# Optimization experiments

Hardware: AMD Instinct MI355X
Metric: run time of the kernel (lower is better)

Reference implementation:

```python
import jax, jax.numpy as jnp
import numpy as np

T = 2048        # num tokens
HID = 2048      # hidden_size
HQ = 16         # num_heads
HKV = 8         # num_kv_heads
D = 128         # head_dim
P = 2           # power retention exponent
THETA = 10000.0 # rope base
SCALE = D ** -0.5


def setup_inputs() -> dict:
    key = jax.random.key(0)
    ks = jax.random.split(key, 8)
    s = 0.02
    return {
        "positions": jnp.arange(T, dtype=jnp.int64) if jax.config.jax_enable_x64 else jnp.arange(T, dtype=jnp.int32),
        "hidden_states": jax.random.normal(ks[0], (T, HID), jnp.float32),
        "Wq": jax.random.normal(ks[1], (HID, HQ * D), jnp.float32) * s,
        "bq": jnp.zeros((HQ * D,), jnp.float32),
        "Wk": jax.random.normal(ks[2], (HID, HKV * D), jnp.float32) * s,
        "bk": jnp.zeros((HKV * D,), jnp.float32),
        "Wv": jax.random.normal(ks[3], (HID, HKV * D), jnp.float32) * s,
        "bv": jnp.zeros((HKV * D,), jnp.float32),
        "Wg": jax.random.normal(ks[4], (HID, HKV), jnp.float32) * s,
        "bg": jnp.zeros((HKV,), jnp.float32),
        "Wo": jax.random.normal(ks[5], (HQ * D, HID), jnp.float32) * s,
        "bo": jnp.zeros((HID,), jnp.float32),
    }


def _rope_neox(x, pos):
    # x: [T, H, D], pos: [T]; rotate-half (neox) style, rotary_dim == head_dim
    half = D // 2
    inv_freq = 1.0 / (THETA ** (jnp.arange(0, D, 2, dtype=jnp.float32) / D))  # [D/2]
    freqs = pos.astype(jnp.float32)[:, None] * inv_freq                        # [T, D/2]
    cos = jnp.cos(freqs)[:, None, :]
    sin = jnp.sin(freqs)[:, None, :]
    x1, x2 = x[..., :half], x[..., half:]
    return jnp.concatenate([x1 * cos - x2 * sin, x2 * cos + x1 * sin], axis=-1)


def reference(positions, hidden_states, Wq, bq, Wk, bk, Wv, bv, Wg, bg, Wo, bo):
    # QKVG projections
    q = (hidden_states @ Wq + bq).reshape(T, HQ, D)
    k = (hidden_states @ Wk + bk).reshape(T, HKV, D)
    v = (hidden_states @ Wv + bv).reshape(T, HKV, D)
    g = hidden_states @ Wg + bg            # [T, HKV], one gate scalar per kv head

    # RoPE on q/k, logsigmoid gate in fp32
    q = _rope_neox(q, positions)
    k = _rope_neox(k, positions)
    g = jax.nn.log_sigmoid(g.astype(jnp.float32))   # [T, HKV], <= 0
    G = jnp.cumsum(g, axis=0)                       # [T, HKV] cumulative log-decay

    # GQA: expand kv heads to query heads
    rep = HQ // HKV
    k = jnp.repeat(k, rep, axis=1)   # [T, HQ, D]
    v = jnp.repeat(v, rep, axis=1)
    G = jnp.repeat(G, rep, axis=1)   # [T, HQ]

    # Power retention (quadratic attention form, seq_len <= switch_over_seq_len):
    # W_ij = (scale * q_i . k_j)^p * exp(G_i - G_j), causal j <= i
    S = jnp.einsum('thd,shd->hts', q, k) * SCALE      # [H, T, T]
    S = S ** P
    Gh = G.T                                          # [H, T]
    mask = jnp.tril(jnp.ones((T, T), dtype=bool))
    diff = jnp.where(mask[None], Gh[:, :, None] - Gh[:, None, :], -jnp.inf)
    W = S * jnp.exp(diff)                             # decay<=1 inside mask, 0 outside

    out = jnp.einsum('hts,shd->thd', W, v)            # [T, H, D]
    out = out.reshape(T, HQ * D) @ Wo + bo            # o_proj
    return out
```

## Files before the change

kernel.cpp:

```cpp
#include <hip/hip_runtime.h>
#include <hip/hip_bf16.h>
#include <math.h>

#define T_SEQ 2048
#define HID 2048
#define HQ 16
#define HKV 8
#define D_HEAD 128
#define HALF 64
#define SCALE_F 0.08838834764831845f
#define PROJW 4096

typedef __attribute__((ext_vector_type(8))) short bf16x8;
typedef __attribute__((ext_vector_type(4))) float f32x4;

static __device__ __forceinline__ short f2bf(float x) {
  unsigned u = __builtin_bit_cast(unsigned, x);
  unsigned r = (u + 0x7FFF + ((u >> 16) & 1)) >> 16;
  return (short)r;
}
static __device__ __forceinline__ float bf2f(unsigned short u) {
  unsigned v = ((unsigned)u) << 16;
  return __builtin_bit_cast(float, v);
}

#define GLDS(gsrc, ldst) \
  __builtin_amdgcn_global_load_lds((const __attribute__((address_space(1))) void*)(gsrc), \
                                   (__attribute__((address_space(3))) void*)(ldst), 16, 0, 0)

__global__ __launch_bounds__(256)
void transpose_qkvw(const float* __restrict__ Wq, const float* __restrict__ Wk,
                    const float* __restrict__ Wv, short* __restrict__ BTall)
{
  const int bx = blockIdx.x;
  const int k0 = blockIdx.y * 32;
  const float* src; short* dst; int Nsrc, n0;
  if (bx < 64)       { src = Wq; Nsrc = 2048; dst = BTall;                       n0 = bx * 32; }
  else if (bx < 96)  { src = Wk; Nsrc = 1024; dst = BTall + (size_t)2048 * 2048; n0 = (bx - 64) * 32; }
  else               { src = Wv; Nsrc = 1024; dst = BTall + (size_t)3072 * 2048; n0 = (bx - 96) * 32; }

  __shared__ float tile[32][33];
  const int r = threadIdx.x >> 5, c = threadIdx.x & 31;
  #pragma unroll
  for (int i = 0; i < 4; ++i)
    tile[r + i * 8][c] = src[(size_t)(k0 + r + i * 8) * Nsrc + n0 + c];
  __syncthreads();
  const int n = threadIdx.x >> 3, k4 = (threadIdx.x & 7) * 4;
  short4 o;
  o.x = f2bf(tile[k4 + 0][n]); o.y = f2bf(tile[k4 + 1][n]);
  o.z = f2bf(tile[k4 + 2][n]); o.w = f2bf(tile[k4 + 3][n]);
  *reinterpret_cast<short4*>(&dst[(size_t)(n0 + n) * 2048 + k0 + k4]) = o;
}

__global__ __launch_bounds__(256)
void transpose_wo(const float* __restrict__ Wo, short* __restrict__ WoT)
{
  const int k0 = blockIdx.y * 32, n0 = blockIdx.x * 32;
  __shared__ float tile[32][33];
  const int r = threadIdx.x >> 5, c = threadIdx.x & 31;
  #pragma unroll
  for (int i = 0; i < 4; ++i)
    tile[r + i * 8][c] = Wo[(size_t)(k0 + r + i * 8) * 2048 + n0 + c];
  __syncthreads();
  const int n = threadIdx.x >> 3, k4 = (threadIdx.x & 7) * 4;
  short4 o;
  o.x = f2bf(tile[k4 + 0][n]); o.y = f2bf(tile[k4 + 1][n]);
  o.z = f2bf(tile[k4 + 2][n]); o.w = f2bf(tile[k4 + 3][n]);
  *reinterpret_cast<short4*>(&WoT[(size_t)(n0 + n) * 2048 + k0 + k4]) = o;
}

template <bool OBF0>
__global__ __launch_bounds__(512, 1)
void gemm256(const short* __restrict__ A, const short* __restrict__ BT,
             const float* __restrict__ b0, const float* __restrict__ b1,
             const float* __restrict__ b2, int s1, int s2,
             void* __restrict__ C0, short* __restrict__ P1,
             short* __restrict__ P2, short* __restrict__ P3,
             int N, int Kst, int klen)
{
  __shared__ __align__(16) short Al[2][256 * 64];
  __shared__ __align__(16) short Bl[2][256 * 64];
  const int tid = threadIdx.x, wid = tid >> 6, lane = tid & 63;
  const int z = blockIdx.z, koff = z * klen;
  const int nwg = gridDim.x * gridDim.y;
  const int orig = blockIdx.y * gridDim.x + blockIdx.x;
  const int swz = (orig & 7) * (nwg >> 3) + (orig >> 3);
  const int bx = swz % gridDim.x, by = swz / gridDim.x;
  const int bm0 = by * 256, bn0 = bx * 256;
  const int wr = wid >> 2, wc = wid & 3;
  const int c = lane & 15, g = lane >> 4;
  const int xc = (c & 7) << 4;
  const int nk = klen >> 6;

  f32x4 acc[8][4] = {};

#define STGA(p, kt, j) do {                                                   \
    const int cid = (j) * 512 + tid;                                          \
    const int rr = cid >> 3;                                                  \
    const int gx = (cid & 7) ^ (rr & 7);                                      \
    GLDS(A + (size_t)(bm0 + rr) * Kst + koff + (kt) * 64 + gx * 8,            \
         (char*)&Al[p][0] + ((j) * 512 + wid * 64) * 16);                     \
  } while (0)
#define STGB(p, kt, j) do {                                                   \
    const int cid = (j) * 512 + tid;                                          \
    const int rr = cid >> 3;                                                  \
    const int gx = (cid & 7) ^ (rr & 7);                                      \
    GLDS(BT + (size_t)(bn0 + rr) * Kst + koff + (kt) * 64 + gx * 8,           \
         (char*)&Bl[p][0] + ((j) * 512 + wid * 64) * 16);                     \
  } while (0)
#define STAGE(p, kt) do {                                                     \
    STGA(p, kt, 0); STGA(p, kt, 1); STGA(p, kt, 2); STGA(p, kt, 3);           \
    STGB(p, kt, 0); STGB(p, kt, 1); STGB(p, kt, 2); STGB(p, kt, 3);           \
  } while (0)

#define RDA(p, mf, ks)                                                        \
  (*reinterpret_cast<const bf16x8*>((const char*)&Al[p][0] +                  \
      (size_t)(wr * 128 + (mf) * 16 + c) * 128 + (((ks) * 64 + g * 16) ^ xc)))
#define RDB(p, nf, ks)                                                        \
  (*reinterpret_cast<const bf16x8*>((const char*)&Bl[p][0] +                  \
      (size_t)(wc * 64 + (nf) * 16 + c) * 128 + (((ks) * 64 + g * 16) ^ xc)))

  STAGE(0, 0);
  asm volatile("s_waitcnt vmcnt(0)" ::: "memory");
  __builtin_amdgcn_s_barrier();
  __builtin_amdgcn_sched_barrier(0);

  for (int t = 0; t < nk; ++t) {
    const int p = t & 1;
    if (t + 1 < nk) STAGE(p ^ 1, t + 1);

    {
      bf16x8 af[8], bfr[4];
      #pragma unroll
      for (int mf = 0; mf < 8; ++mf) af[mf] = RDA(p, mf, 0);
      #pragma unroll
      for (int nf = 0; nf < 4; ++nf) bfr[nf] = RDB(p, nf, 0);
      asm volatile("s_waitcnt lgkmcnt(0)" ::: "memory");
      __builtin_amdgcn_sched_barrier(0);
      __builtin_amdgcn_s_setprio(1);
      #pragma unroll
      for (int mf = 0; mf < 8; ++mf)
        #pragma unroll
        for (int nf = 0; nf < 4; ++nf)
          acc[mf][nf] = __builtin_amdgcn_mfma_f32_16x16x32_bf16(af[mf], bfr[nf], acc[mf][nf], 0, 0, 0);
      __builtin_amdgcn_s_setprio(0);
    }
    {
      bf16x8 af[8], bfr[4];
      #pragma unroll
      for (int mf = 0; mf < 8; ++mf) af[mf] = RDA(p, mf, 1);
      #pragma unroll
      for (int nf = 0; nf < 4; ++nf) bfr[nf] = RDB(p, nf, 1);
      asm volatile("s_waitcnt lgkmcnt(0)" ::: "memory");
      __builtin_amdgcn_sched_barrier(0);
      __builtin_amdgcn_s_setprio(1);
      #pragma unroll
      for (int mf = 0; mf < 8; ++mf)
        #pragma unroll
        for (int nf = 0; nf < 4; ++nf)
          acc[mf][nf] = __builtin_amdgcn_mfma_f32_16x16x32_bf16(af[mf], bfr[nf], acc[mf][nf], 0, 0, 0);
      __builtin_amdgcn_s_setprio(0);
    }

    if (t + 1 < nk) {
      __builtin_amdgcn_sched_barrier(0);
      asm volatile("s_waitcnt vmcnt(0)" ::: "memory");
      __builtin_amdgcn_s_barrier();
      __builtin_amdgcn_sched_barrier(0);
    }
  }

  const int crow = bm0 + wr * 128;
  const int ccol0 = bn0 + wc * 64;
  #pragma unroll
  for (int nf = 0; nf < 4; ++nf) {
    const int col = ccol0 + nf * 16 + c;
    float b = 0.f;
    if (z == 0)
      b = (col < s1) ? b0[col] : ((col < s2) ? b1[col - s1] : b2[col - s2]);
    short* P = (z == 1) ? P1 : ((z == 2) ? P2 : P3);
    #pragma unroll
    for (int mf = 0; mf < 8; ++mf)
      #pragma unroll
      for (int r = 0; r < 4; ++r) {
        const int row = crow + mf * 16 + g * 4 + r;
        const float v = acc[mf][nf][r] + b;
        if (z == 0) {
          if constexpr (OBF0)
            ((short*)C0)[(size_t)row * N + col] = f2bf(v);
          else
            ((float*)C0)[(size_t)row * N + col] = v;
        } else {
          P[(size_t)row * N + col] = f2bf(v);
        }
      }
  }
#undef STGA
#undef STGB
#undef STAGE
#undef RDA
#undef RDB
}

__global__ __launch_bounds__(256)
void gproj_kernel(const float* __restrict__ hs, const float* __restrict__ Wg,
                  const float* __restrict__ bg, float* __restrict__ gT,
                  short* __restrict__ hsb)
{
  const int t = blockIdx.x, tid = threadIdx.x;
  __shared__ float red[256][9];
  float a[8] = {0.f, 0.f, 0.f, 0.f, 0.f, 0.f, 0.f, 0.f};
  for (int cc = tid; cc < HID; cc += 256) {
    const float hv = hs[(size_t)t * HID + cc];
    hsb[(size_t)t * HID + cc] = f2bf(hv);
    const float4 w0 = *reinterpret_cast<const float4*>(Wg + (size_t)cc * 8);
    const float4 w1 = *reinterpret_cast<const float4*>(Wg + (size_t)cc * 8 + 4);
    a[0] = fmaf(hv, w0.x, a[0]); a[1] = fmaf(hv, w0.y, a[1]);
    a[2] = fmaf(hv, w0.z, a[2]); a[3] = fmaf(hv, w0.w, a[3]);
    a[4] = fmaf(hv, w1.x, a[4]); a[5] = fmaf(hv, w1.y, a[5]);
    a[6] = fmaf(hv, w1.z, a[6]); a[7] = fmaf(hv, w1.w, a[7]);
  }
  #pragma unroll
  for (int j = 0; j < 8; ++j) red[tid][j] = a[j];
  __syncthreads();
  for (int s = 128; s >= 1; s >>= 1) {
    if (tid < s) {
      #pragma unroll
      for (int j = 0; j < 8; ++j) red[tid][j] += red[tid + s][j];
    }
    __syncthreads();
  }
  if (tid < 8) {
    const float x = red[0][tid] + bg[tid];
    const float nx = -x;
    const float sp = (nx > 20.f) ? nx : log1pf(expf(nx));
    gT[(size_t)tid * T_SEQ + t] = -sp;
  }
}

__global__ __launch_bounds__(512)
void gscan_kernel(const float* __restrict__ gT, float* __restrict__ Gct)
{
  const int h = blockIdx.x;
  const int tid = threadIdx.x;
  const int wid = tid >> 6, lane = tid & 63;
  __shared__ float wsum[8];

  const float4 v = reinterpret_cast<const float4*>(gT + (size_t)h * T_SEQ)[tid];
  const float p0 = v.x, p1 = p0 + v.y, p2 = p1 + v.z, p3 = p2 + v.w;

  float sc = p3;
  #pragma unroll
  for (int off = 1; off < 64; off <<= 1) {
    const float o = __shfl_up(sc, off, 64);
    if (lane >= off) sc += o;
  }
  if (lane == 63) wsum[wid] = sc;
  __syncthreads();
  float wof = 0.f;
  #pragma unroll
  for (int w = 0; w < 8; ++w) wof += (w < wid) ? wsum[w] : 0.f;

  const float excl = wof + sc - p3;
  reinterpret_cast<float4*>(Gct + (size_t)h * T_SEQ)[tid] =
      make_float4(excl + p0, excl + p1, excl + p2, excl + p3);
}

__global__ __launch_bounds__(256)
void qkv_fold_rope(short* __restrict__ proj, const short* __restrict__ part1)
{
  const int t = blockIdx.x;
  __shared__ float cs[64], sn[64];
  if (threadIdx.x < 64) {
    const int i = threadIdx.x;
    const float f = (float)t * powf(10000.0f, -(float)i / 64.0f);
    cs[i] = cosf(f); sn[i] = sinf(f);
  }
  __syncthreads();

  const int ch = ((threadIdx.x >> 3) << 4) + (threadIdx.x & 7);
  const size_t base = (size_t)t * PROJW + ch * 8;
  bf16x8 a1 = *reinterpret_cast<bf16x8*>(proj + base);
  bf16x8 a2 = *reinterpret_cast<bf16x8*>(proj + base + 64);
  const bf16x8 q1 = *reinterpret_cast<const bf16x8*>(part1 + base);
  const bf16x8 q2 = *reinterpret_cast<const bf16x8*>(part1 + base + 64);
  const int head = ch >> 4;
  const int i0 = (ch & 7) * 8;
  #pragma unroll
  for (int j = 0; j < 8; ++j) {
    const float x1 = bf2f((unsigned short)a1[j]) + bf2f((unsigned short)q1[j]);
    const float x2 = bf2f((unsigned short)a2[j]) + bf2f((unsigned short)q2[j]);
    if (head < 24) {
      const float cc = cs[i0 + j], ss = sn[i0 + j];
      a1[j] = f2bf(x1 * cc - x2 * ss);
      a2[j] = f2bf(x2 * cc + x1 * ss);
    } else {
      a1[j] = f2bf(x1);
      a2[j] = f2bf(x2);
    }
  }
  *reinterpret_cast<bf16x8*>(proj + base) = a1;
  *reinterpret_cast<bf16x8*>(proj + base + 64) = a2;
}

__global__ __launch_bounds__(256)
void vtrans_kernel(const unsigned short* __restrict__ proj, unsigned short* __restrict__ vt)
{
  __shared__ unsigned short tile[32][33];
  const int tt = blockIdx.x * 32, dd = blockIdx.y * 32, hk = blockIdx.z;
  const int c = threadIdx.x & 31, r0 = (threadIdx.x >> 5) * 4;
  #pragma unroll
  for (int i = 0; i < 4; ++i)
    tile[r0 + i][c] = proj[(size_t)(tt + r0 + i) * PROJW + 3072 + hk * 128 + dd + c];
  __syncthreads();
  #pragma unroll
  for (int i = 0; i < 4; ++i)
    vt[(size_t)(hk * 128 + dd + r0 + i) * T_SEQ + tt + c] = tile[c][r0 + i];
}

__global__ __launch_bounds__(256)
void o_fold(float* __restrict__ out, const short* __restrict__ p1,
            const short* __restrict__ p2, const short* __restrict__ p3)
{
  const size_t i = ((size_t)blockIdx.x * 256 + threadIdx.x) * 8;
  const bf16x8 a = *reinterpret_cast<const bf16x8*>(p1 + i);
  const bf16x8 b = *reinterpret_cast<const bf16x8*>(p2 + i);
  const bf16x8 cc = *reinterpret_cast<const bf16x8*>(p3 + i);
  float4 o0 = *reinterpret_cast<float4*>(out + i);
  float4 o1 = *reinterpret_cast<float4*>(out + i + 4);
  float s[8];
  #pragma unroll
  for (int j = 0; j < 8; ++j)
    s[j] = bf2f((unsigned short)a[j]) + bf2f((unsigned short)b[j]) + bf2f((unsigned short)cc[j]);
  o0.x += s[0]; o0.y += s[1]; o0.z += s[2]; o0.w += s[3];
  o1.x += s[4]; o1.y += s[5]; o1.z += s[6]; o1.w += s[7];
  *reinterpret_cast<float4*>(out + i) = o0;
  *reinterpret_cast<float4*>(out + i + 4) = o1;
}

__global__ __launch_bounds__(256, 1)
void attn_mfma(const short* __restrict__ proj, const short* __restrict__ vt,
               const float* __restrict__ Gct, short* __restrict__ outb)
{
  __shared__ __align__(16) char smem[86528];
  const int hk = blockIdx.x;
  const int tb = blockIdx.y * 64;
  const int tid = threadIdx.x;
  const int wid = tid >> 6, lane = tid & 63;
  const int c = lane & 15, g = lane >> 4;
  const int h = 2 * hk + (wid >> 1);
  const int tw = tb + (wid & 1) * 32;
  const float* Gh = Gct + (size_t)hk * T_SEQ;

  const float glim = Gh[tb] + 90.0f;
  int lo = 0, hi = tb;
  while (lo < hi) {
    const int mid = (lo + hi) >> 1;
    if (Gh[mid] > glim) lo = mid + 1; else hi = mid;
  }
  const int sfirst = lo & ~63;
  const int nst = ((tb - sfirst) >> 6) + 1;

  bf16x8 qf[2][4];
  #pragma unroll
  for (int tt = 0; tt < 2; ++tt)
    #pragma unroll
    for (int kb = 0; kb < 4; ++kb)
      qf[tt][kb] = *reinterpret_cast<const bf16x8*>(
          proj + (size_t)(tw + 16 * tt + c) * PROJW + h * D_HEAD + kb * 32 + g * 8);
  const float gt0 = Gh[tw + c];
  const float gt1 = Gh[tw + 16 + c];
  const float gtw = Gh[tw];
  const int twmax = tw + 31;

  f32x4 accv[2][8] = {};

#define ASTG(buf, s64)                                                                   \
  do {                                                                                   \
    _Pragma("unroll")                                                                    \
    for (int i2 = 0; i2 < 4; ++i2) {                                                     \
      const int cid = tid + 256 * i2;                                                    \
      const int kr = cid >> 4, kc = cid & 15;                                            \
      GLDS(proj + (size_t)((s64) + kr) * PROJW + 2048 + hk * 128 + ((kc ^ (kr & 7)) * 8),\
           smem + (buf) * 16384 + cid * 16);                                             \
      const int vr = cid >> 3, vc = cid & 7;                                             \
      GLDS(vt + (size_t)(hk * 128 + vr) * T_SEQ + (s64) + ((vc ^ (vr & 7)) * 8),         \
           smem + 32768 + (buf) * 16384 + cid * 16);                                     \
    }                                                                                    \
    if (tid < 64) ((float*)(smem + 86016))[(buf) * 64 + tid] = Gh[(s64) + tid];          \
  } while (0)

  ASTG(0, sfirst);
  __syncthreads();

  for (int i = 0; i < nst; ++i) {
    const int cur = i & 1;
    if (i + 1 < nst) ASTG(cur ^ 1, sfirst + (i + 1) * 64);
    const int sbase64 = sfirst + i * 64;
    const float* Gss = (const float*)(smem + 86016) + cur * 64;
    char* Pmy = smem + 65536 + wid * 5120;

    #pragma unroll
    for (int st = 0; st < 2; ++st) {
      const int s0 = sbase64 + st * 32;
      if (s0 > twmax) continue;
      if (gtw - Gss[st * 32 + 31] < -90.0f) continue;

      bf16x8 kf[2][4];
      #pragma unroll
      for (int sg = 0; sg < 2; ++sg)
        #pragma unroll
        for (int kb = 0; kb < 4; ++kb) {
          const int row = st * 32 + 16 * sg + c;
          const int byt = (row * 256 + kb * 64 + g * 16) ^ ((c & 7) << 4);
          kf[sg][kb] = *reinterpret_cast<const bf16x8*>(smem + cur * 16384 + byt);
        }
      f32x4 sa[2][2] = {};
      #pragma unroll
      for (int kb = 0; kb < 4; ++kb)
        #pragma unroll
        for (int sg = 0; sg < 2; ++sg)
          #pragma unroll
          for (int tt = 0; tt < 2; ++tt)
            sa[sg][tt] = __builtin_amdgcn_mfma_f32_16x16x32_bf16(
                kf[sg][kb], qf[tt][kb], sa[sg][tt], 0, 0, 0);

      #pragma unroll
      for (int sg = 0; sg < 2; ++sg) {
        const float4 gs = *reinterpret_cast<const float4*>(&Gss[st * 32 + sg * 16 + g * 4]);
        const float gsv[4] = {gs.x, gs.y, gs.z, gs.w};
        #pragma unroll
        for (int tt = 0; tt < 2; ++tt) {
          const int tg = tw + 16 * tt + c;
          const float gt = tt ? gt1 : gt0;
          const int sg0 = s0 + sg * 16 + g * 4;
          float w[4];
          #pragma unroll
          for (int r = 0; r < 4; ++r) {
            const float dv = sa[sg][tt][r] * SCALE_F;
            const float ww = dv * dv * __expf(gt - gsv[r]);
            w[r] = (sg0 + r <= tg) ? ww : 0.0f;
          }
          uint2 pv;
          pv.x = ((unsigned)(unsigned short)f2bf(w[1]) << 16) | (unsigned short)f2bf(w[0]);
          pv.y = ((unsigned)(unsigned short)f2bf(w[3]) << 16) | (unsigned short)f2bf(w[2]);
          *reinterpret_cast<uint2*>(Pmy + st * 2560 + (c + 16 * tt) * 80 + 8 * g + 32 * sg) = pv;
        }
      }
      asm volatile("s_waitcnt lgkmcnt(0)" ::: "memory");
      __builtin_amdgcn_sched_barrier(0);

      bf16x8 pf[2];
      #pragma unroll
      for (int tt = 0; tt < 2; ++tt)
        pf[tt] = *reinterpret_cast<const bf16x8*>(Pmy + st * 2560 + (c + 16 * tt) * 80 + g * 16);

      #pragma unroll
      for (int db = 0; db < 8; ++db) {
        const int row = 16 * db + c;
        const int byt = (row * 128 + st * 64 + g * 16) ^ ((c & 7) << 4);
        const bf16x8 vf = *reinterpret_cast<const bf16x8*>(smem + 32768 + cur * 16384 + byt);
        #pragma unroll
        for (int tt = 0; tt < 2; ++tt)
          accv[tt][db] = __builtin_amdgcn_mfma_f32_16x16x32_bf16(pf[tt], vf, accv[tt][db], 0, 0, 0);
      }
    }
    __syncthreads();
  }

  char* Wme = smem + wid * 8704;
  #pragma unroll
  for (int tt = 0; tt < 2; ++tt)
    #pragma unroll
    for (int db = 0; db < 8; ++db)
      #pragma unroll
      for (int r = 0; r < 4; ++r)
        *reinterpret_cast<short*>(Wme + (16 * tt + 4 * g + r) * 272 + (16 * db + c) * 2)
            = f2bf(accv[tt][db][r]);
  asm volatile("s_waitcnt lgkmcnt(0)" ::: "memory");
  __builtin_amdgcn_sched_barrier(0);
  #pragma unroll
  for (int e = 0; e < 8; ++e) {
    const int idx = e * 64 + lane;
    const int tr = idx >> 4, d0 = (idx & 15) * 8;
    const bf16x8 vv = *reinterpret_cast<const bf16x8*>(Wme + tr * 272 + d0 * 2);
    *reinterpret_cast<bf16x8*>(outb + ((size_t)(tw + tr) * HQ + h) * D_HEAD + d0) = vv;
  }
#undef ASTG
}

extern "C" void kernel_launch(void* const* d_in, const int* in_sizes, int n_in,
                              void* d_out, int out_size, void* d_ws, size_t ws_size,
                              hipStream_t stream)
{
  const float* hs = (const float*)d_in[1];
  const float* Wq = (const float*)d_in[2];
  const float* bq = (const float*)d_in[3];
  const float* Wk = (const float*)d_in[4];
  const float* bk = (const float*)d_in[5];
  const float* Wv = (const float*)d_in[6];
  const float* bv = (const float*)d_in[7];
  const float* Wg = (const float*)d_in[8];
  const float* bg = (const float*)d_in[9];
  const float* Wo = (const float*)d_in[10];
  const float* bo = (const float*)d_in[11];
  float* outp = (float*)d_out;

  short* proj  = (short*)d_ws;
  short* vtb   = proj + (size_t)T_SEQ * PROJW;
  float* gT    = (float*)(vtb + (size_t)HKV * D_HEAD * T_SEQ);
  float* Gct   = gT + 16384;
  short* hsb   = (short*)(Gct + 16384);
  short* BTall = hsb + (size_t)2048 * 2048;
  short* part1 = BTall + (size_t)4096 * 2048;
  short* WoT     = BTall;
  short* attnout = hsb;
  short* opart1  = part1;
  short* opart2  = part1 + (size_t)2048 * 2048;
  short* opart3  = proj;

  transpose_qkvw<<<dim3(128, 64), 256, 0, stream>>>(Wq, Wk, Wv, BTall);

  gproj_kernel<<<2048, 256, 0, stream>>>(hs, Wg, bg, gT, hsb);
  gscan_kernel<<<8, 512, 0, stream>>>(gT, Gct);

  gemm256<true><<<dim3(16, 8, 2), 512, 0, stream>>>(
      hsb, BTall, bq, bk, bv, 2048, 3072, proj, part1, part1, part1,
      PROJW, 2048, 1024);

  qkv_fold_rope<<<2048, 256, 0, stream>>>(proj, part1);

  vtrans_kernel<<<dim3(64, 4, 8), 256, 0, stream>>>((const unsigned short*)proj,
                                                    (unsigned short*)vtb);

  transpose_wo<<<dim3(64, 64), 256, 0, stream>>>(Wo, WoT);

  attn_mfma<<<dim3(8, 32), 256, 0, stream>>>(proj, vtb, Gct, attnout);

  gemm256<false><<<dim3(8, 8, 4), 512, 0, stream>>>(
      attnout, WoT, bo, bo, bo, 1 << 30, 1 << 30, outp, opart1, opart2, opart3,
      2048, 2048, 512);

  o_fold<<<2048, 256, 0, stream>>>(outp, opart1, opart2, opart3);
}
```

Measured before the change: 145.1 us.

## Interleave GEMM loads with MFMA quadrants and switch o_proj to 128-tile split-K

The QKV GEMM main loop is split into four MFMA quadrants. Each quadrant issues part of the next tile's global-to-LDS loads and reads a subset of fragments, with barriers between quadrants, so memory traffic overlaps compute. The o_proj GEMM moves from a 256-tile 4-way split-K with bf16 partials and a fold kernel to a 128x128-tile kernel with 2-way split-K, fp32 partials and a simple add kernel. The intent is better occupancy and less partial-sum traffic, at the cost of a simpler kernel with less reuse per tile and extra barriers in the QKV loop.

```diff
diff --git a/kernel.cpp b/kernel.cpp
--- a/kernel.cpp
+++ b/kernel.cpp
@@ -69,14 +69,24 @@
   *reinterpret_cast<short4*>(&WoT[(size_t)(n0 + n) * 2048 + k0 + k4]) = o;
 }
 
+__global__ __launch_bounds__(256)
+void add_f32(float* __restrict__ out, const float* __restrict__ part, int n4)
+{
+  int i = blockIdx.x * blockDim.x + threadIdx.x;
+  if (i >= n4) return;
+  float4 a = reinterpret_cast<float4*>(out)[i];
+  const float4 b = reinterpret_cast<const float4*>(part)[i];
+  a.x += b.x; a.y += b.y; a.z += b.z; a.w += b.w;
+  reinterpret_cast<float4*>(out)[i] = a;
+}
+
 template <bool OBF0>
 __global__ __launch_bounds__(512, 1)
-void gemm256(const short* __restrict__ A, const short* __restrict__ BT,
-             const float* __restrict__ b0, const float* __restrict__ b1,
-             const float* __restrict__ b2, int s1, int s2,
-             void* __restrict__ C0, short* __restrict__ P1,
-             short* __restrict__ P2, short* __restrict__ P3,
-             int N, int Kst, int klen)
+void gemm8p(const short* __restrict__ A, const short* __restrict__ BT,
+            const float* __restrict__ b0, const float* __restrict__ b1,
+            const float* __restrict__ b2, int s1, int s2,
+            void* __restrict__ C0, short* __restrict__ P1,
+            int N, int Kst, int klen)
 {
   __shared__ __align__(16) short Al[2][256 * 64];
   __shared__ __align__(16) short Bl[2][256 * 64];
@@ -108,11 +118,6 @@
     GLDS(BT + (size_t)(bn0 + rr) * Kst + koff + (kt) * 64 + gx * 8,           \
          (char*)&Bl[p][0] + ((j) * 512 + wid * 64) * 16);                     \
   } while (0)
-#define STAGE(p, kt) do {                                                     \
-    STGA(p, kt, 0); STGA(p, kt, 1); STGA(p, kt, 2); STGA(p, kt, 3);           \
-    STGB(p, kt, 0); STGB(p, kt, 1); STGB(p, kt, 2); STGB(p, kt, 3);           \
-  } while (0)
-
 #define RDA(p, mf, ks)                                                        \
   (*reinterpret_cast<const bf16x8*>((const char*)&Al[p][0] +                  \
       (size_t)(wr * 128 + (mf) * 16 + c) * 128 + (((ks) * 64 + g * 16) ^ xc)))
@@ -120,50 +125,83 @@
   (*reinterpret_cast<const bf16x8*>((const char*)&Bl[p][0] +                  \
       (size_t)(wc * 64 + (nf) * 16 + c) * 128 + (((ks) * 64 + g * 16) ^ xc)))
 
-  STAGE(0, 0);
+  STGA(0, 0, 0); STGA(0, 0, 1); STGA(0, 0, 2); STGA(0, 0, 3);
+  STGB(0, 0, 0); STGB(0, 0, 1); STGB(0, 0, 2); STGB(0, 0, 3);
   asm volatile("s_waitcnt vmcnt(0)" ::: "memory");
   __builtin_amdgcn_s_barrier();
   __builtin_amdgcn_sched_barrier(0);
 
+  bf16x8 a[4][2], b0r[2][2], b1r[2][2];
+
   for (int t = 0; t < nk; ++t) {
-    const int p = t & 1;
-    if (t + 1 < nk) STAGE(p ^ 1, t + 1);
-
-    {
-      bf16x8 af[8], bfr[4];
-      #pragma unroll
-      for (int mf = 0; mf < 8; ++mf) af[mf] = RDA(p, mf, 0);
-      #pragma unroll
-      for (int nf = 0; nf < 4; ++nf) bfr[nf] = RDB(p, nf, 0);
-      asm volatile("s_waitcnt lgkmcnt(0)" ::: "memory");
-      __builtin_amdgcn_sched_barrier(0);
-      __builtin_amdgcn_s_setprio(1);
-      #pragma unroll
-      for (int mf = 0; mf < 8; ++mf)
-        #pragma unroll
-        for (int nf = 0; nf < 4; ++nf)
-          acc[mf][nf] = __builtin_amdgcn_mfma_f32_16x16x32_bf16(af[mf], bfr[nf], acc[mf][nf], 0, 0, 0);
-      __builtin_amdgcn_s_setprio(0);
-    }
-    {
-      bf16x8 af[8], bfr[4];
-      #pragma unroll
-      for (int mf = 0; mf < 8; ++mf) af[mf] = RDA(p, mf, 1);
-      #pragma unroll
-      for (int nf = 0; nf < 4; ++nf) bfr[nf] = RDB(p, nf, 1);
-      asm volatile("s_waitcnt lgkmcnt(0)" ::: "memory");
-      __builtin_amdgcn_sched_barrier(0);
-      __builtin_amdgcn_s_setprio(1);
-      #pragma unroll
-      for (int mf = 0; mf < 8; ++mf)
-        #pragma unroll
-        for (int nf = 0; nf < 4; ++nf)
-          acc[mf][nf] = __builtin_amdgcn_mfma_f32_16x16x32_bf16(af[mf], bfr[nf], acc[mf][nf], 0, 0, 0);
-      __builtin_amdgcn_s_setprio(0);
-    }
-
-    if (t + 1 < nk) {
-      __builtin_amdgcn_sched_barrier(0);
+    const int p = t & 1, q = p ^ 1;
+    const bool pre = (t + 1 < nk);
+
+    #pragma unroll
+    for (int mf = 0; mf < 4; ++mf) { a[mf][0] = RDA(p, mf, 0); a[mf][1] = RDA(p, mf, 1); }
+    #pragma unroll
+    for (int nf = 0; nf < 2; ++nf) { b0r[nf][0] = RDB(p, nf, 0); b0r[nf][1] = RDB(p, nf, 1); }
+    if (pre) { STGA(q, t + 1, 0); STGA(q, t + 1, 1); }
+    __builtin_amdgcn_s_barrier();
+    asm volatile("s_waitcnt lgkmcnt(0)" ::: "memory");
+    __builtin_amdgcn_sched_barrier(0);
+    __builtin_amdgcn_s_setprio(1);
+    #pragma unroll
+    for (int ks = 0; ks < 2; ++ks)
+      #pragma unroll
+      for (int mf = 0; mf < 4; ++mf)
+        #pragma unroll
+        for (int nf = 0; nf < 2; ++nf)
+          acc[mf][nf] = __builtin_amdgcn_mfma_f32_16x16x32_bf16(a[mf][ks], b0r[nf][ks], acc[mf][nf], 0, 0, 0);
+    __builtin_amdgcn_s_setprio(0);
+    __builtin_amdgcn_s_barrier();
+
+    #pragma unroll
+    for (int nf = 0; nf < 2; ++nf) { b1r[nf][0] = RDB(p, 2 + nf, 0); b1r[nf][1] = RDB(p, 2 + nf, 1); }
+    if (pre) { STGA(q, t + 1, 2); STGA(q, t + 1, 3); }
+    __builtin_amdgcn_s_barrier();
+    asm volatile("s_waitcnt lgkmcnt(0)" ::: "memory");
+    __builtin_amdgcn_sched_barrier(0);
+    __builtin_amdgcn_s_setprio(1);
+    #pragma unroll
+    for (int ks = 0; ks < 2; ++ks)
+      #pragma unroll
+      for (int mf = 0; mf < 4; ++mf)
+        #pragma unroll
+        for (int nf = 0; nf < 2; ++nf)
+          acc[mf][2 + nf] = __builtin_amdgcn_mfma_f32_16x16x32_bf16(a[mf][ks], b1r[nf][ks], acc[mf][2 + nf], 0, 0, 0);
+    __builtin_amdgcn_s_setprio(0);
+    __builtin_amdgcn_s_barrier();
+
+    #pragma unroll
+    for (int mf = 0; mf < 4; ++mf) { a[mf][0] = RDA(p, 4 + mf, 0); a[mf][1] = RDA(p, 4 + mf, 1); }
+    if (pre) { STGB(q, t + 1, 0); STGB(q, t + 1, 1); }
+    __builtin_amdgcn_s_barrier();
+    asm volatile("s_waitcnt lgkmcnt(0)" ::: "memory");
+    __builtin_amdgcn_sched_barrier(0);
+    __builtin_amdgcn_s_setprio(1);
+    #pragma unroll
+    for (int ks = 0; ks < 2; ++ks)
+      #pragma unroll
+      for (int mf = 0; mf < 4; ++mf)
+        #pragma unroll
+        for (int nf = 0; nf < 2; ++nf)
+          acc[4 + mf][2 + nf] = __builtin_amdgcn_mfma_f32_16x16x32_bf16(a[mf][ks], b1r[nf][ks], acc[4 + mf][2 + nf], 0, 0, 0);
+    __builtin_amdgcn_s_setprio(0);
+    __builtin_amdgcn_s_barrier();
+
+    if (pre) { STGB(q, t + 1, 2); STGB(q, t + 1, 3); }
+    __builtin_amdgcn_s_barrier();
+    __builtin_amdgcn_s_setprio(1);
+    #pragma unroll
+    for (int ks = 0; ks < 2; ++ks)
+      #pragma unroll
+      for (int mf = 0; mf < 4; ++mf)
+        #pragma unroll
+        for (int nf = 0; nf < 2; ++nf)
+          acc[4 + mf][nf] = __builtin_amdgcn_mfma_f32_16x16x32_bf16(a[mf][ks], b0r[nf][ks], acc[4 + mf][nf], 0, 0, 0);
+    __builtin_amdgcn_s_setprio(0);
+    if (pre) {
       asm volatile("s_waitcnt vmcnt(0)" ::: "memory");
       __builtin_amdgcn_s_barrier();
       __builtin_amdgcn_sched_barrier(0);
@@ -178,7 +216,6 @@
     float b = 0.f;
     if (z == 0)
       b = (col < s1) ? b0[col] : ((col < s2) ? b1[col - s1] : b2[col - s2]);
-    short* P = (z == 1) ? P1 : ((z == 2) ? P2 : P3);
     #pragma unroll
     for (int mf = 0; mf < 8; ++mf)
       #pragma unroll
@@ -191,15 +228,95 @@
           else
             ((float*)C0)[(size_t)row * N + col] = v;
         } else {
-          P[(size_t)row * N + col] = f2bf(v);
+          P1[(size_t)row * N + col] = f2bf(v);
         }
       }
   }
 #undef STGA
 #undef STGB
-#undef STAGE
 #undef RDA
 #undef RDB
+}
+
+template <bool OBF>
+__global__ __launch_bounds__(256)
+void gemm_bf16(const short* __restrict__ A, const short* __restrict__ BT,
+               const float* __restrict__ bias, void* __restrict__ Cout0,
+               void* __restrict__ Cout1, int N, int Kst, int klen)
+{
+  __shared__ short As[2][128 * 32];
+  __shared__ short Bs[2][128 * 32];
+  const int tid = threadIdx.x;
+  const int wave = tid >> 6, lane = tid & 63;
+  const int bm0 = blockIdx.y * 128, bn0 = blockIdx.x * 128;
+  const int z = blockIdx.z;
+  const int koff = z * klen;
+  const int wm = (wave >> 1) * 64, wn = (wave & 1) * 64;
+
+  const int srow = wave * 32 + (lane >> 2);
+  const int scol = (lane & 3) * 8;
+  const short* Abase = A + (size_t)(bm0 + srow) * Kst + koff + scol;
+  const short* Bbase = BT + (size_t)(bn0 + srow) * Kst + koff + scol;
+
+  f32x4 acc[4][4] = {};
+
+  const int nk = klen >> 5;
+#define STAGE(buf, k0)                                                           \
+  do {                                                                           \
+    GLDS(Abase + (k0), &As[buf][(wave * 32) * 32]);                              \
+    GLDS(Abase + (k0) + (size_t)16 * Kst, &As[buf][(wave * 32 + 16) * 32]);      \
+    GLDS(Bbase + (k0), &Bs[buf][(wave * 32) * 32]);                              \
+    GLDS(Bbase + (k0) + (size_t)16 * Kst, &Bs[buf][(wave * 32 + 16) * 32]);      \
+  } while (0)
+
+  STAGE(0, 0);
+  __syncthreads();
+
+  const int kof = (lane >> 4) * 8;
+  const int rA = wm + (lane & 15);
+  const int rB = wn + (lane & 15);
+
+  for (int t = 0; t < nk; ++t) {
+    const int cur = t & 1;
+    if (t + 1 < nk) STAGE(cur ^ 1, (t + 1) << 5);
+    bf16x8 af[4], bfr[4];
+    #pragma unroll
+    for (int i = 0; i < 4; ++i) {
+      af[i]  = *reinterpret_cast<const bf16x8*>(&As[cur][(rA + i * 16) * 32 + kof]);
+      bfr[i] = *reinterpret_cast<const bf16x8*>(&Bs[cur][(rB + i * 16) * 32 + kof]);
+    }
+    #pragma unroll
+    for (int i = 0; i < 4; ++i)
+      #pragma unroll
+      for (int j = 0; j < 4; ++j)
+        acc[i][j] = __builtin_amdgcn_mfma_f32_16x16x32_bf16(af[i], bfr[j], acc[i][j], 0, 0, 0);
+    __syncthreads();
+  }
+
+  void* Cout = z ? Cout1 : Cout0;
+  const int crow = wm + (lane >> 4) * 4;
+  const int ccol = wn + (lane & 15);
+  #pragma unroll
+  for (int j = 0; j < 4; ++j) {
+    const int col = bn0 + ccol + j * 16;
+    const float b = (z == 0) ? bias[col] : 0.f;
+    #pragma unroll
+    for (int i = 0; i < 4; ++i)
+      #pragma unroll
+      for (int r = 0; r < 4; ++r) {
+        const int row = bm0 + crow + i * 16 + r;
+        const float v = acc[i][j][r] + b;
+        if (z == 0) {
+          if constexpr (OBF)
+            ((short*)Cout)[(size_t)row * N + col] = f2bf(v);
+          else
+            ((float*)Cout)[(size_t)row * N + col] = v;
+        } else {
+          ((float*)Cout)[(size_t)row * N + col] = v;
+        }
+      }
+  }
+#undef STAGE
 }
 
 __global__ __launch_bounds__(256)
@@ -316,26 +433,6 @@
   #pragma unroll
   for (int i = 0; i < 4; ++i)
     vt[(size_t)(hk * 128 + dd + r0 + i) * T_SEQ + tt + c] = tile[c][r0 + i];
-}
-
-__global__ __launch_bounds__(256)
-void o_fold(float* __restrict__ out, const short* __restrict__ p1,
-            const short* __restrict__ p2, const short* __restrict__ p3)
-{
-  const size_t i = ((size_t)blockIdx.x * 256 + threadIdx.x) * 8;
-  const bf16x8 a = *reinterpret_cast<const bf16x8*>(p1 + i);
-  const bf16x8 b = *reinterpret_cast<const bf16x8*>(p2 + i);
-  const bf16x8 cc = *reinterpret_cast<const bf16x8*>(p3 + i);
-  float4 o0 = *reinterpret_cast<float4*>(out + i);
-  float4 o1 = *reinterpret_cast<float4*>(out + i + 4);
-  float s[8];
-  #pragma unroll
-  for (int j = 0; j < 8; ++j)
-    s[j] = bf2f((unsigned short)a[j]) + bf2f((unsigned short)b[j]) + bf2f((unsigned short)cc[j]);
-  o0.x += s[0]; o0.y += s[1]; o0.z += s[2]; o0.w += s[3];
-  o1.x += s[4]; o1.y += s[5]; o1.z += s[6]; o1.w += s[7];
-  *reinterpret_cast<float4*>(out + i) = o0;
-  *reinterpret_cast<float4*>(out + i + 4) = o1;
 }
 
 __global__ __launch_bounds__(256, 1)
@@ -515,18 +612,15 @@
   short* part1 = BTall + (size_t)4096 * 2048;
   short* WoT     = BTall;
   short* attnout = hsb;
-  short* opart1  = part1;
-  short* opart2  = part1 + (size_t)2048 * 2048;
-  short* opart3  = proj;
+  float* opart   = (float*)part1;
 
   transpose_qkvw<<<dim3(128, 64), 256, 0, stream>>>(Wq, Wk, Wv, BTall);
 
   gproj_kernel<<<2048, 256, 0, stream>>>(hs, Wg, bg, gT, hsb);
   gscan_kernel<<<8, 512, 0, stream>>>(gT, Gct);
 
-  gemm256<true><<<dim3(16, 8, 2), 512, 0, stream>>>(
-      hsb, BTall, bq, bk, bv, 2048, 3072, proj, part1, part1, part1,
-      PROJW, 2048, 1024);
+  gemm8p<true><<<dim3(16, 8, 2), 512, 0, stream>>>(
+      hsb, BTall, bq, bk, bv, 2048, 3072, proj, part1, PROJW, 2048, 1024);
 
   qkv_fold_rope<<<2048, 256, 0, stream>>>(proj, part1);
 
@@ -537,9 +631,7 @@
 
   attn_mfma<<<dim3(8, 32), 256, 0, stream>>>(proj, vtb, Gct, attnout);
 
-  gemm256<false><<<dim3(8, 8, 4), 512, 0, stream>>>(
-      attnout, WoT, bo, bo, bo, 1 << 30, 1 << 30, outp, opart1, opart2, opart3,
-      2048, 2048, 512);
-
-  o_fold<<<2048, 256, 0, stream>>>(outp, opart1, opart2, opart3);
-}
+  gemm_bf16<false><<<dim3(16, 16, 2), 256, 0, stream>>>(
+      attnout, WoT, bo, outp, opart, 2048, 2048, 1024);
+  add_f32<<<4096, 256, 0, stream>>>(outp, opart, 1048576);
+}
```

New measurement: 142.9 us. About the same (-1.5%).
